# Kernel tuning notes

Hardware: AMD Instinct MI355X
Metric: run time of the kernel (lower is better)

The kernel has to match this reference:

```python
import jax, jax.numpy as jnp
import numpy as np

B, N, D_OBS, D_MSG, H = 4096, 64, 128, 64, 4
HD = D_MSG // H
EPS = 1e-5


def setup_inputs() -> dict:
    key = jax.random.key(0)
    ks = jax.random.split(key, 16)
    def w(k, shape):
        fan_in = shape[0]
        return (jax.random.normal(k, shape, dtype=jnp.float32) / np.sqrt(fan_in)).astype(jnp.float32)
    return {
        'obs_all': jax.random.normal(ks[0], (B, N, D_OBS), dtype=jnp.float32),
        # msg encoder: Linear(obs,128) -> ReLU -> Linear(128,msg)
        'enc_w1': w(ks[1], (D_OBS, 128)), 'enc_b1': jnp.zeros((128,), jnp.float32),
        'enc_w2': w(ks[2], (128, D_MSG)), 'enc_b2': jnp.zeros((D_MSG,), jnp.float32),
        # MultiheadAttention in/out projections (stored as (in, out))
        'in_proj_w': w(ks[3], (D_MSG, 3 * D_MSG)), 'in_proj_b': jnp.zeros((3 * D_MSG,), jnp.float32),
        'out_w': w(ks[4], (D_MSG, D_MSG)), 'out_b': jnp.zeros((D_MSG,), jnp.float32),
        # integrator: Linear(obs+msg,256) -> LayerNorm(256) -> ReLU -> Linear(256,obs)
        'int_w1': w(ks[5], (D_OBS + D_MSG, 256)), 'int_b1': jnp.zeros((256,), jnp.float32),
        'ln_g': jnp.ones((256,), jnp.float32), 'ln_b': jnp.zeros((256,), jnp.float32),
        'int_w2': w(ks[6], (256, D_OBS)), 'int_b2': jnp.zeros((D_OBS,), jnp.float32),
    }


def reference(obs_all, enc_w1, enc_b1, enc_w2, enc_b2,
              in_proj_w, in_proj_b, out_w, out_b,
              int_w1, int_b1, ln_g, ln_b, int_w2, int_b2):
    # --- send: encode observations into messages (B, N, msg_dim) ---
    h = jax.nn.relu(obs_all @ enc_w1 + enc_b1)
    msgs = h @ enc_w2 + enc_b2

    # --- attention aggregation: per-agent query over all messages.
    # The original per-agent loop (query = msgs[:, i:i+1]) is exactly
    # batched self-attention over the agent axis.
    qkv = msgs @ in_proj_w + in_proj_b            # (B, N, 3*msg)
    q, k, v = jnp.split(qkv, 3, axis=-1)
    q = q.reshape(B, N, H, HD)
    k = k.reshape(B, N, H, HD)
    v = v.reshape(B, N, H, HD)
    scale = 1.0 / np.sqrt(HD)
    scores = jnp.einsum('bqhd,bkhd->bhqk', q, k) * scale   # (B, H, N, N)
    attn = jax.nn.softmax(scores, axis=-1)
    ctx = jnp.einsum('bhqk,bkhd->bqhd', attn, v).reshape(B, N, D_MSG)
    agg = ctx @ out_w + out_b                     # (B, N, msg_dim)

    # --- receive: concat obs + aggregated message, MLP with LayerNorm ---
    combined = jnp.concatenate([obs_all, agg], axis=-1)
    z = combined @ int_w1 + int_b1                # (B, N, 256)
    mu = jnp.mean(z, axis=-1, keepdims=True)
    var = jnp.var(z, axis=-1, keepdims=True)
    z = (z - mu) * jax.lax.rsqrt(var + EPS) * ln_g + ln_b
    enriched = jax.nn.relu(z) @ int_w2 + int_b2   # (B, N, obs_dim)
    return enriched, msgs
```

## Files before the change

### kernel.cpp

```cpp
#include <hip/hip_runtime.h>


typedef __attribute__((ext_vector_type(8))) short bf16x8;
typedef __attribute__((ext_vector_type(4))) float f32x4;
typedef __attribute__((ext_vector_type(16))) float f32x16;

#define MFMA16(a, b, c) __builtin_amdgcn_mfma_f32_16x16x32_bf16((a), (b), (c), 0, 0, 0)
#define MFMA32(a, b, c) __builtin_amdgcn_mfma_f32_32x32x16_bf16((a), (b), (c), 0, 0, 0)

__device__ __forceinline__ float b2f(short s) {
    union { unsigned u; float f; } x;
    x.u = ((unsigned)(unsigned short)s) << 16;
    return x.f;
}
__device__ __forceinline__ short f2b(float f) {
    union { float f; unsigned u; } x;
    x.f = f;
    unsigned r = (x.u + 0x7FFFu + ((x.u >> 16) & 1u)) >> 16;
    return (short)r;
}

template<bool F32>
__device__ __forceinline__ float ldS(const void* p, int i) {
    if (F32) return ((const float*)p)[i];
    return b2f(((const short*)p)[i]);
}
template<bool F32>
__device__ __forceinline__ bf16x8 ld8(const void* p, long i) {
    if (F32) {
        const float4* f = (const float4*)((const float*)p + i);
        float4 a = f[0], b = f[1];
        bf16x8 r;
        r[0] = f2b(a.x); r[1] = f2b(a.y); r[2] = f2b(a.z); r[3] = f2b(a.w);
        r[4] = f2b(b.x); r[5] = f2b(b.y); r[6] = f2b(b.z); r[7] = f2b(b.w);
        return r;
    }
    return *(const bf16x8*)((const short*)p + i);
}
template<bool F32>
__device__ __forceinline__ void st(void* p, long i, float v) {
    if (F32) ((float*)p)[i] = v;
    else ((short*)p)[i] = f2b(v);
}

#define P_S   0
#define H_S   0
#define Z_S   0
#define Q2_S  9216
#define AG_S  9216
#define K2_S  13312
#define VT_S  17408
#define LN_S  17408
#define MU_S  18432
#define MS_S  22016
#define SMEM_SHORTS 26624
#define HP 136
#define MP 72
#define ZP 264
#define PP 72
#define VP 72

#define WT1_OFF   0
#define WT2_OFF   16384
#define WTQ_OFF   24576
#define WTO_OFF   36864
#define WTI1_OFF  40960
#define WTI2_OFF  90112

__global__ void detect_dtype(const unsigned short* __restrict__ obs, int* __restrict__ flag) {
    if (blockIdx.x != 0) return;
    int lane = threadIdx.x & 63;
    int cnt = 0;
    for (int i = lane; i < 512; i += 64) {
        unsigned e = (obs[i] >> 7) & 0xFFu;
        cnt += (e == 0u || (e >= 80u && e <= 140u)) ? 1 : 0;
    }
#pragma unroll
    for (int off = 1; off < 64; off <<= 1) cnt += __shfl_xor(cnt, off);
    if (lane == 0) *flag = (cnt >= 480) ? 1 : 0;
}

__global__ void wtrans(const void* __restrict__ w1, const void* __restrict__ w2,
                       const void* __restrict__ wq, const void* __restrict__ wo,
                       const void* __restrict__ wi1, const void* __restrict__ wi2,
                       const int* __restrict__ flag, short* __restrict__ wt) {
    const bool f32 = (*flag == 0);
    int id = blockIdx.x * 256 + threadIdx.x;
    const void* src;
    int K, N, off, loc;
    if (id < 16384)       { src = w1;  K = 128; N = 128; off = WT1_OFF;  loc = id; }
    else if (id < 24576)  { src = w2;  K = 128; N = 64;  off = WT2_OFF;  loc = id - 16384; }
    else if (id < 36864)  { src = wq;  K = 64;  N = 192; off = WTQ_OFF;  loc = id - 24576; }
    else if (id < 40960)  { src = wo;  K = 64;  N = 64;  off = WTO_OFF;  loc = id - 36864; }
    else if (id < 90112)  { src = wi1; K = 192; N = 256; off = WTI1_OFF; loc = id - 40960; }
    else if (id < 122880) { src = wi2; K = 256; N = 128; off = WTI2_OFF; loc = id - 90112; }
    else return;
    int n = loc / K;
    int k = loc - n * K;
    float v = f32 ? ((const float*)src)[k * N + n] : b2f(((const short*)src)[k * N + n]);
    wt[off + loc] = f2b(v);
}

template<bool F32>
__global__ __launch_bounds__(256, 3)
void macs_main(const void* __restrict__ obs,
               const void* __restrict__ eb1, const void* __restrict__ eb2,
               const void* __restrict__ ipb, const void* __restrict__ ob,
               const void* __restrict__ ib1, const void* __restrict__ lg,
               const void* __restrict__ lb,  const void* __restrict__ ib2,
               const int* __restrict__ flag, const short* __restrict__ wt,
               void* __restrict__ out) {
    if (*flag != (F32 ? 0 : 1)) return;
    __shared__ __align__(16) short smem[SMEM_SHORTS];
    const int tid = threadIdx.x;
    const int w = tid >> 6;
    const int lane = tid & 63;
    const int q = lane >> 4;
    const int t = lane & 15;
    const int l31 = lane & 31;
    const int hi = lane >> 5;
    const int b = blockIdx.x;
    const long obase = (long)b * 64 * 128;

    {
        f32x4 acc[4][2] = {};
        const short* wt1 = wt + WT1_OFF;
#pragma unroll
        for (int ks = 0; ks < 4; ++ks) {
            bf16x8 a[4], bb[2];
#pragma unroll
            for (int mt = 0; mt < 4; ++mt)
                a[mt] = ld8<F32>(obs, obase + (mt * 16 + t) * 128 + ks * 32 + q * 8);
#pragma unroll
            for (int tj = 0; tj < 2; ++tj)
                bb[tj] = *(const bf16x8*)(wt1 + (w * 32 + tj * 16 + t) * 128 + ks * 32 + q * 8);
#pragma unroll
            for (int mt = 0; mt < 4; ++mt)
#pragma unroll
                for (int tj = 0; tj < 2; ++tj)
                    acc[mt][tj] = MFMA16(a[mt], bb[tj], acc[mt][tj]);
        }
        short* hs = smem + H_S;
#pragma unroll
        for (int tj = 0; tj < 2; ++tj) {
            int c = w * 32 + tj * 16 + t;
            float bias = ldS<F32>(eb1, c);
#pragma unroll
            for (int mt = 0; mt < 4; ++mt)
#pragma unroll
                for (int i = 0; i < 4; ++i) {
                    int r = mt * 16 + q * 4 + i;
                    hs[r * HP + c] = f2b(fmaxf(acc[mt][tj][i] + bias, 0.f));
                }
        }
    }
    __syncthreads();

    {
        f32x4 acc[4] = {};
        const short* wt2 = wt + WT2_OFF;
        const short* hs = smem + H_S;
#pragma unroll
        for (int ks = 0; ks < 4; ++ks) {
            bf16x8 a[4];
            bf16x8 bb = *(const bf16x8*)(wt2 + (w * 16 + t) * 128 + ks * 32 + q * 8);
#pragma unroll
            for (int mt = 0; mt < 4; ++mt)
                a[mt] = *(const bf16x8*)(hs + (mt * 16 + t) * HP + ks * 32 + q * 8);
#pragma unroll
            for (int mt = 0; mt < 4; ++mt)
                acc[mt] = MFMA16(a[mt], bb, acc[mt]);
        }
        short* ms = smem + MS_S;
        float bias = ldS<F32>(eb2, w * 16 + t);
        const long msgs_base = 33554432L;
#pragma unroll
        for (int mt = 0; mt < 4; ++mt)
#pragma unroll
            for (int i = 0; i < 4; ++i) {
                int r = mt * 16 + q * 4 + i;
                float v = acc[mt][i] + bias;
                ms[r * MP + w * 16 + t] = f2b(v);
                st<F32>(out, msgs_base + ((long)b * 64 + r) * 64 + w * 16 + t, v);
            }
    }
    __syncthreads();

    {
        f32x4 acc[4][3] = {};
        const short* wtq = wt + WTQ_OFF;
        const short* ms = smem + MS_S;
#pragma unroll
        for (int ks = 0; ks < 2; ++ks) {
            bf16x8 a[4], bb[3];
#pragma unroll
            for (int mt = 0; mt < 4; ++mt)
                a[mt] = *(const bf16x8*)(ms + (mt * 16 + t) * MP + ks * 32 + q * 8);
#pragma unroll
            for (int tj = 0; tj < 3; ++tj)
                bb[tj] = *(const bf16x8*)(wtq + (w * 48 + tj * 16 + t) * 64 + ks * 32 + q * 8);
#pragma unroll
            for (int mt = 0; mt < 4; ++mt)
#pragma unroll
                for (int tj = 0; tj < 3; ++tj)
                    acc[mt][tj] = MFMA16(a[mt], bb[tj], acc[mt][tj]);
        }
#pragma unroll
        for (int tj = 0; tj < 3; ++tj) {
            int c = w * 48 + tj * 16 + t;
            float bias = ldS<F32>(ipb, c);
            int sec = c >> 6;
            int head = (c >> 4) & 3;
            float scale = (sec == 0) ? 0.25f : 1.0f;
#pragma unroll
            for (int mt = 0; mt < 4; ++mt)
#pragma unroll
                for (int i = 0; i < 4; ++i) {
                    int r = mt * 16 + q * 4 + i;
                    short bv = f2b((acc[mt][tj][i] + bias) * scale);
                    int idx;
                    if (sec == 0)      idx = Q2_S + head * 1024 + r * 16 + t;
                    else if (sec == 1) idx = K2_S + head * 1024 + r * 16 + t;
                    else               idx = VT_S + head * 1152 + t * VP + r;
                    smem[idx] = bv;
                }
        }
    }
    __syncthreads();

    {
        const int rh = w & 1;
        short* Pq = smem + P_S + w * 2304;
        short* cs = smem + MS_S;
#pragma unroll
        for (int p = 0; p < 2; ++p) {
            const int hd = p * 2 + (w >> 1);
            const short* qh = smem + Q2_S + hd * 1024;
            const short* kh = smem + K2_S + hd * 1024;
            const short* vh = smem + VT_S + hd * 1152;
            f32x16 sc0 = {}, sc1 = {};
            {
                bf16x8 aq  = *(const bf16x8*)(qh + (rh * 32 + l31) * 16 + hi * 8);
                bf16x8 bk0 = *(const bf16x8*)(kh + l31 * 16 + hi * 8);
                bf16x8 bk1 = *(const bf16x8*)(kh + (32 + l31) * 16 + hi * 8);
                sc0 = MFMA32(aq, bk0, sc0);
                sc1 = MFMA32(aq, bk1, sc1);
            }
#pragma unroll
            for (int i = 0; i < 16; ++i) {
                int lr = (i & 3) + 8 * (i >> 2) + 4 * hi;
                float e0 = __expf(sc0[i]);
                float e1 = __expf(sc1[i]);
                float s = e0 + e1;
#pragma unroll
                for (int off = 1; off < 32; off <<= 1) s += __shfl_xor(s, off);
                float inv = 1.f / s;
                Pq[lr * PP + l31]      = f2b(e0 * inv);
                Pq[lr * PP + 32 + l31] = f2b(e1 * inv);
            }
            f32x4 cx[2] = {};
#pragma unroll
            for (int ks = 0; ks < 2; ++ks) {
                bf16x8 bb = *(const bf16x8*)(vh + t * VP + ks * 32 + q * 8);
                bf16x8 a0 = *(const bf16x8*)(Pq + t * PP + ks * 32 + q * 8);
                bf16x8 a1 = *(const bf16x8*)(Pq + (16 + t) * PP + ks * 32 + q * 8);
                cx[0] = MFMA16(a0, bb, cx[0]);
                cx[1] = MFMA16(a1, bb, cx[1]);
            }
#pragma unroll
            for (int mt = 0; mt < 2; ++mt)
#pragma unroll
                for (int i = 0; i < 4; ++i)
                    cs[(rh * 32 + mt * 16 + q * 4 + i) * MP + hd * 16 + t] = f2b(cx[mt][i]);
        }
    }
    __syncthreads();

    {
        f32x4 acc[4] = {};
        const short* wto = wt + WTO_OFF;
        const short* cs = smem + MS_S;
#pragma unroll
        for (int ks = 0; ks < 2; ++ks) {
            bf16x8 a[4];
            bf16x8 bb = *(const bf16x8*)(wto + (w * 16 + t) * 64 + ks * 32 + q * 8);
#pragma unroll
            for (int mt = 0; mt < 4; ++mt)
                a[mt] = *(const bf16x8*)(cs + (mt * 16 + t) * MP + ks * 32 + q * 8);
#pragma unroll
            for (int mt = 0; mt < 4; ++mt)
                acc[mt] = MFMA16(a[mt], bb, acc[mt]);
        }
        short* ag = smem + AG_S;
        float bias = ldS<F32>(ob, w * 16 + t);
#pragma unroll
        for (int mt = 0; mt < 4; ++mt)
#pragma unroll
            for (int i = 0; i < 4; ++i)
                ag[(mt * 16 + q * 4 + i) * MP + w * 16 + t] = f2b(acc[mt][i] + bias);
    }
    __syncthreads();

    {
        f32x4 acc[4][4] = {};
        const short* wti1 = wt + WTI1_OFF;
        const short* ag = smem + AG_S;
#pragma unroll
        for (int ks = 0; ks < 6; ++ks) {
            bf16x8 a[4], bb[4];
            if (ks < 4) {
#pragma unroll
                for (int mt = 0; mt < 4; ++mt)
                    a[mt] = ld8<F32>(obs, obase + (mt * 16 + t) * 128 + ks * 32 + q * 8);
            } else {
#pragma unroll
                for (int mt = 0; mt < 4; ++mt)
                    a[mt] = *(const bf16x8*)(ag + (mt * 16 + t) * MP + (ks - 4) * 32 + q * 8);
            }
#pragma unroll
            for (int tj = 0; tj < 4; ++tj)
                bb[tj] = *(const bf16x8*)(wti1 + (w * 64 + tj * 16 + t) * 192 + ks * 32 + q * 8);
#pragma unroll
            for (int mt = 0; mt < 4; ++mt)
#pragma unroll
                for (int tj = 0; tj < 4; ++tj)
                    acc[mt][tj] = MFMA16(a[mt], bb[tj], acc[mt][tj]);
        }
#pragma unroll
        for (int tj = 0; tj < 4; ++tj) {
            float bias = ldS<F32>(ib1, w * 64 + tj * 16 + t);
#pragma unroll
            for (int mt = 0; mt < 4; ++mt)
#pragma unroll
                for (int i = 0; i < 4; ++i) acc[mt][tj][i] += bias;
        }
        float2* lnred = (float2*)(smem + LN_S);
#pragma unroll
        for (int mt = 0; mt < 4; ++mt)
#pragma unroll
            for (int i = 0; i < 4; ++i) {
                float s = 0.f, s2 = 0.f;
#pragma unroll
                for (int tj = 0; tj < 4; ++tj) {
                    float v = acc[mt][tj][i];
                    s += v;
                    s2 += v * v;
                }
#pragma unroll
                for (int off = 1; off < 16; off <<= 1) {
                    s += __shfl_xor(s, off);
                    s2 += __shfl_xor(s2, off);
                }
                if (t == 0) {
                    float2 p; p.x = s; p.y = s2;
                    lnred[(mt * 16 + q * 4 + i) * 4 + w] = p;
                }
            }
        __syncthreads();
        float2* munr = (float2*)(smem + MU_S);
        if (tid < 64) {
            float S = 0.f, S2 = 0.f;
#pragma unroll
            for (int j = 0; j < 4; ++j) {
                float2 p = lnred[tid * 4 + j];
                S += p.x;
                S2 += p.y;
            }
            float mu = S * (1.f / 256.f);
            float var = S2 * (1.f / 256.f) - mu * mu;
            float2 m; m.x = mu; m.y = rsqrtf(fmaxf(var, 0.f) + 1e-5f);
            munr[tid] = m;
        }
        __syncthreads();
        short* zs = smem + Z_S;
        float gv[4], bv[4];
#pragma unroll
        for (int tj = 0; tj < 4; ++tj) {
            gv[tj] = ldS<F32>(lg, w * 64 + tj * 16 + t);
            bv[tj] = ldS<F32>(lb, w * 64 + tj * 16 + t);
        }
#pragma unroll
        for (int mt = 0; mt < 4; ++mt)
#pragma unroll
            for (int i = 0; i < 4; ++i) {
                int r = mt * 16 + q * 4 + i;
                float2 mr = munr[r];
#pragma unroll
                for (int tj = 0; tj < 4; ++tj) {
                    float v = (acc[mt][tj][i] - mr.x) * mr.y * gv[tj] + bv[tj];
                    zs[r * ZP + w * 64 + tj * 16 + t] = f2b(fmaxf(v, 0.f));
                }
            }
    }
    __syncthreads();

    {
        f32x4 acc[4][2] = {};
        const short* wti2 = wt + WTI2_OFF;
        const short* zs = smem + Z_S;
#pragma unroll
        for (int ks = 0; ks < 8; ++ks) {
            bf16x8 a[4], bb[2];
#pragma unroll
            for (int mt = 0; mt < 4; ++mt)
                a[mt] = *(const bf16x8*)(zs + (mt * 16 + t) * ZP + ks * 32 + q * 8);
#pragma unroll
            for (int tj = 0; tj < 2; ++tj)
                bb[tj] = *(const bf16x8*)(wti2 + (w * 32 + tj * 16 + t) * 256 + ks * 32 + q * 8);
#pragma unroll
            for (int mt = 0; mt < 4; ++mt)
#pragma unroll
                for (int tj = 0; tj < 2; ++tj)
                    acc[mt][tj] = MFMA16(a[mt], bb[tj], acc[mt][tj]);
        }
#pragma unroll
        for (int tj = 0; tj < 2; ++tj) {
            int c = w * 32 + tj * 16 + t;
            float bias = ldS<F32>(ib2, c);
#pragma unroll
            for (int mt = 0; mt < 4; ++mt)
#pragma unroll
                for (int i = 0; i < 4; ++i) {
                    int r = mt * 16 + q * 4 + i;
                    st<F32>(out, ((long)b * 64 + r) * 128 + c, acc[mt][tj][i] + bias);
                }
        }
    }
}

extern "C" void kernel_launch(void* const* d_in, const int* in_sizes, int n_in,
                              void* d_out, int out_size, void* d_ws, size_t ws_size,
                              hipStream_t stream) {
    const void* obs = d_in[0];
    const void* w1  = d_in[1];
    const void* b1  = d_in[2];
    const void* w2  = d_in[3];
    const void* b2  = d_in[4];
    const void* wq  = d_in[5];
    const void* bq  = d_in[6];
    const void* wo  = d_in[7];
    const void* bo  = d_in[8];
    const void* wi1 = d_in[9];
    const void* bi1 = d_in[10];
    const void* lg  = d_in[11];
    const void* lb  = d_in[12];
    const void* wi2 = d_in[13];
    const void* bi2 = d_in[14];
    int* flag = (int*)d_ws;
    short* wt = (short*)d_ws + 128;

    detect_dtype<<<dim3(1), dim3(64), 0, stream>>>((const unsigned short*)obs, flag);
    wtrans<<<dim3(480), dim3(256), 0, stream>>>(w1, w2, wq, wo, wi1, wi2, flag, wt);
    macs_main<false><<<dim3(4096), dim3(256), 0, stream>>>(obs, b1, b2, bq, bo, bi1, lg, lb, bi2, flag, wt, d_out);
    macs_main<true ><<<dim3(4096), dim3(256), 0, stream>>>(obs, b1, b2, bq, bo, bi1, lg, lb, bi2, flag, wt, d_out);
}
```

Measured before the change: 582.5 us.

## Pre-convert fp32 obs to bf16 in workspace, fuse prep kernels, hoist weight loads

Merges dtype detection and weight transposition into one prep kernel, which can also convert the fp32 observation tensor to bf16 in workspace when the workspace is large enough. The main kernel then reads bf16 obs, halving obs traffic on its two reads. It also hoists weight and obs fragment loads ahead of the MFMA loops so more loads are in flight. The trade-off is an extra full pass that reads obs once and writes a bf16 copy, plus higher register pressure under 3-wave occupancy bounds. The conversion path only runs when ws_size is big enough.

```diff
diff --git a/kernel.cpp b/kernel.cpp
--- a/kernel.cpp
+++ b/kernel.cpp
@@ -36,6 +36,11 @@
         return r;
     }
     return *(const bf16x8*)((const short*)p + i);
+}
+template<bool F32, bool OBSBF>
+__device__ __forceinline__ bf16x8 ldobs(const void* obs, const short* obs_bf, long i) {
+    if (OBSBF) return *(const bf16x8*)(obs_bf + i);
+    return ld8<F32>(obs, i);
 }
 template<bool F32>
 __device__ __forceinline__ void st(void* p, long i, float v) {
@@ -66,42 +71,57 @@
 #define WTO_OFF   36864
 #define WTI1_OFF  40960
 #define WTI2_OFF  90112
-
-__global__ void detect_dtype(const unsigned short* __restrict__ obs, int* __restrict__ flag) {
-    if (blockIdx.x != 0) return;
+#define WT_TOTAL  122880
+#define OBS_ELEMS 33554432L
+#define WS_NEEDED (256UL + (unsigned long)WT_TOTAL * 2 + (unsigned long)OBS_ELEMS * 2)
+
+template<bool DO_CONV>
+__global__ void prep(const void* __restrict__ obs,
+                     const void* __restrict__ w1, const void* __restrict__ w2,
+                     const void* __restrict__ wq, const void* __restrict__ wo,
+                     const void* __restrict__ wi1, const void* __restrict__ wi2,
+                     int* __restrict__ flag, short* __restrict__ wt,
+                     short* __restrict__ obs_bf) {
+    const unsigned short* o16 = (const unsigned short*)obs;
     int lane = threadIdx.x & 63;
     int cnt = 0;
     for (int i = lane; i < 512; i += 64) {
-        unsigned e = (obs[i] >> 7) & 0xFFu;
+        unsigned e = (o16[i] >> 7) & 0xFFu;
         cnt += (e == 0u || (e >= 80u && e <= 140u)) ? 1 : 0;
     }
 #pragma unroll
     for (int off = 1; off < 64; off <<= 1) cnt += __shfl_xor(cnt, off);
-    if (lane == 0) *flag = (cnt >= 480) ? 1 : 0;
-}
-
-__global__ void wtrans(const void* __restrict__ w1, const void* __restrict__ w2,
-                       const void* __restrict__ wq, const void* __restrict__ wo,
-                       const void* __restrict__ wi1, const void* __restrict__ wi2,
-                       const int* __restrict__ flag, short* __restrict__ wt) {
-    const bool f32 = (*flag == 0);
-    int id = blockIdx.x * 256 + threadIdx.x;
-    const void* src;
-    int K, N, off, loc;
-    if (id < 16384)       { src = w1;  K = 128; N = 128; off = WT1_OFF;  loc = id; }
-    else if (id < 24576)  { src = w2;  K = 128; N = 64;  off = WT2_OFF;  loc = id - 16384; }
-    else if (id < 36864)  { src = wq;  K = 64;  N = 192; off = WTQ_OFF;  loc = id - 24576; }
-    else if (id < 40960)  { src = wo;  K = 64;  N = 64;  off = WTO_OFF;  loc = id - 36864; }
-    else if (id < 90112)  { src = wi1; K = 192; N = 256; off = WTI1_OFF; loc = id - 40960; }
-    else if (id < 122880) { src = wi2; K = 256; N = 128; off = WTI2_OFF; loc = id - 90112; }
-    else return;
-    int n = loc / K;
-    int k = loc - n * K;
-    float v = f32 ? ((const float*)src)[k * N + n] : b2f(((const short*)src)[k * N + n]);
-    wt[off + loc] = f2b(v);
-}
-
-template<bool F32>
+    const bool isbf16 = (cnt >= 480);
+    if (blockIdx.x == 0 && threadIdx.x == 0) *flag = isbf16 ? 1 : 0;
+
+    long id = (long)blockIdx.x * 256 + threadIdx.x;
+    if (id < WT_TOTAL) {
+        const void* src;
+        int K, N, off, loc = (int)id;
+        if (loc < 16384)      { src = w1;  K = 128; N = 128; off = WT1_OFF; }
+        else if (loc < 24576) { src = w2;  K = 128; N = 64;  off = WT2_OFF;  loc -= 16384; }
+        else if (loc < 36864) { src = wq;  K = 64;  N = 192; off = WTQ_OFF;  loc -= 24576; }
+        else if (loc < 40960) { src = wo;  K = 64;  N = 64;  off = WTO_OFF;  loc -= 36864; }
+        else if (loc < 90112) { src = wi1; K = 192; N = 256; off = WTI1_OFF; loc -= 40960; }
+        else                  { src = wi2; K = 256; N = 128; off = WTI2_OFF; loc -= 90112; }
+        int n = loc / K;
+        int k = loc - n * K;
+        float v = isbf16 ? b2f(((const short*)src)[k * N + n]) : ((const float*)src)[k * N + n];
+        wt[off + loc] = f2b(v);
+    } else if (DO_CONV && !isbf16) {
+        long base = (id - WT_TOTAL) * 8;
+        if (base < OBS_ELEMS) {
+            const float4* f = (const float4*)((const float*)obs + base);
+            float4 a = f[0], b = f[1];
+            bf16x8 r;
+            r[0] = f2b(a.x); r[1] = f2b(a.y); r[2] = f2b(a.z); r[3] = f2b(a.w);
+            r[4] = f2b(b.x); r[5] = f2b(b.y); r[6] = f2b(b.z); r[7] = f2b(b.w);
+            *(bf16x8*)(obs_bf + base) = r;
+        }
+    }
+}
+
+template<bool F32, bool OBSBF>
 __global__ __launch_bounds__(256, 3)
 void macs_main(const void* __restrict__ obs,
                const void* __restrict__ eb1, const void* __restrict__ eb2,
@@ -109,7 +129,7 @@
                const void* __restrict__ ib1, const void* __restrict__ lg,
                const void* __restrict__ lb,  const void* __restrict__ ib2,
                const int* __restrict__ flag, const short* __restrict__ wt,
-               void* __restrict__ out) {
+               const short* __restrict__ obs_bf, void* __restrict__ out) {
     if (*flag != (F32 ? 0 : 1)) return;
     __shared__ __align__(16) short smem[SMEM_SHORTS];
     const int tid = threadIdx.x;
@@ -123,14 +143,17 @@
     const long obase = (long)b * 64 * 128;
 
     {
+        bf16x8 oa[4][4];
+#pragma unroll
+        for (int ks = 0; ks < 4; ++ks)
+#pragma unroll
+            for (int mt = 0; mt < 4; ++mt)
+                oa[ks][mt] = ldobs<F32, OBSBF>(obs, obs_bf, obase + (mt * 16 + t) * 128 + ks * 32 + q * 8);
         f32x4 acc[4][2] = {};
         const short* wt1 = wt + WT1_OFF;
 #pragma unroll
         for (int ks = 0; ks < 4; ++ks) {
-            bf16x8 a[4], bb[2];
-#pragma unroll
-            for (int mt = 0; mt < 4; ++mt)
-                a[mt] = ld8<F32>(obs, obase + (mt * 16 + t) * 128 + ks * 32 + q * 8);
+            bf16x8 bb[2];
 #pragma unroll
             for (int tj = 0; tj < 2; ++tj)
                 bb[tj] = *(const bf16x8*)(wt1 + (w * 32 + tj * 16 + t) * 128 + ks * 32 + q * 8);
@@ -138,7 +161,7 @@
             for (int mt = 0; mt < 4; ++mt)
 #pragma unroll
                 for (int tj = 0; tj < 2; ++tj)
-                    acc[mt][tj] = MFMA16(a[mt], bb[tj], acc[mt][tj]);
+                    acc[mt][tj] = MFMA16(oa[ks][mt], bb[tj], acc[mt][tj]);
         }
         short* hs = smem + H_S;
 #pragma unroll
@@ -157,19 +180,22 @@
     __syncthreads();
 
     {
+        bf16x8 bbv[4];
+        const short* wt2 = wt + WT2_OFF;
+#pragma unroll
+        for (int ks = 0; ks < 4; ++ks)
+            bbv[ks] = *(const bf16x8*)(wt2 + (w * 16 + t) * 128 + ks * 32 + q * 8);
         f32x4 acc[4] = {};
-        const short* wt2 = wt + WT2_OFF;
         const short* hs = smem + H_S;
 #pragma unroll
         for (int ks = 0; ks < 4; ++ks) {
             bf16x8 a[4];
-            bf16x8 bb = *(const bf16x8*)(wt2 + (w * 16 + t) * 128 + ks * 32 + q * 8);
 #pragma unroll
             for (int mt = 0; mt < 4; ++mt)
                 a[mt] = *(const bf16x8*)(hs + (mt * 16 + t) * HP + ks * 32 + q * 8);
 #pragma unroll
             for (int mt = 0; mt < 4; ++mt)
-                acc[mt] = MFMA16(a[mt], bb, acc[mt]);
+                acc[mt] = MFMA16(a[mt], bbv[ks], acc[mt]);
         }
         short* ms = smem + MS_S;
         float bias = ldS<F32>(eb2, w * 16 + t);
@@ -187,23 +213,26 @@
     __syncthreads();
 
     {
+        bf16x8 bbv[6];
+        const short* wtq = wt + WTQ_OFF;
+#pragma unroll
+        for (int ks = 0; ks < 2; ++ks)
+#pragma unroll
+            for (int tj = 0; tj < 3; ++tj)
+                bbv[ks * 3 + tj] = *(const bf16x8*)(wtq + (w * 48 + tj * 16 + t) * 64 + ks * 32 + q * 8);
         f32x4 acc[4][3] = {};
-        const short* wtq = wt + WTQ_OFF;
         const short* ms = smem + MS_S;
 #pragma unroll
         for (int ks = 0; ks < 2; ++ks) {
-            bf16x8 a[4], bb[3];
+            bf16x8 a[4];
 #pragma unroll
             for (int mt = 0; mt < 4; ++mt)
                 a[mt] = *(const bf16x8*)(ms + (mt * 16 + t) * MP + ks * 32 + q * 8);
 #pragma unroll
-            for (int tj = 0; tj < 3; ++tj)
-                bb[tj] = *(const bf16x8*)(wtq + (w * 48 + tj * 16 + t) * 64 + ks * 32 + q * 8);
-#pragma unroll
             for (int mt = 0; mt < 4; ++mt)
 #pragma unroll
                 for (int tj = 0; tj < 3; ++tj)
-                    acc[mt][tj] = MFMA16(a[mt], bb[tj], acc[mt][tj]);
+                    acc[mt][tj] = MFMA16(a[mt], bbv[ks * 3 + tj], acc[mt][tj]);
         }
 #pragma unroll
         for (int tj = 0; tj < 3; ++tj) {
@@ -276,20 +305,29 @@
     }
     __syncthreads();
 
-    {
+    bf16x8 oa6[4][4];
+    {
+#pragma unroll
+        for (int ks = 0; ks < 4; ++ks)
+#pragma unroll
+            for (int mt = 0; mt < 4; ++mt)
+                oa6[ks][mt] = ldobs<F32, OBSBF>(obs, obs_bf, obase + (mt * 16 + t) * 128 + ks * 32 + q * 8);
+        bf16x8 bbv[2];
+        const short* wto = wt + WTO_OFF;
+#pragma unroll
+        for (int ks = 0; ks < 2; ++ks)
+            bbv[ks] = *(const bf16x8*)(wto + (w * 16 + t) * 64 + ks * 32 + q * 8);
         f32x4 acc[4] = {};
-        const short* wto = wt + WTO_OFF;
         const short* cs = smem + MS_S;
 #pragma unroll
         for (int ks = 0; ks < 2; ++ks) {
             bf16x8 a[4];
-            bf16x8 bb = *(const bf16x8*)(wto + (w * 16 + t) * 64 + ks * 32 + q * 8);
 #pragma unroll
             for (int mt = 0; mt < 4; ++mt)
                 a[mt] = *(const bf16x8*)(cs + (mt * 16 + t) * MP + ks * 32 + q * 8);
 #pragma unroll
             for (int mt = 0; mt < 4; ++mt)
-                acc[mt] = MFMA16(a[mt], bb, acc[mt]);
+                acc[mt] = MFMA16(a[mt], bbv[ks], acc[mt]);
         }
         short* ag = smem + AG_S;
         float bias = ldS<F32>(ob, w * 16 + t);
@@ -311,7 +349,7 @@
             if (ks < 4) {
 #pragma unroll
                 for (int mt = 0; mt < 4; ++mt)
-                    a[mt] = ld8<F32>(obs, obase + (mt * 16 + t) * 128 + ks * 32 + q * 8);
+                    a[mt] = oa6[ks][mt];
             } else {
 #pragma unroll
                 for (int mt = 0; mt < 4; ++mt)
@@ -395,23 +433,26 @@
     __syncthreads();
 
     {
+        bf16x8 bbv[8][2];
+        const short* wti2 = wt + WTI2_OFF;
+#pragma unroll
+        for (int ks = 0; ks < 8; ++ks)
+#pragma unroll
+            for (int tj = 0; tj < 2; ++tj)
+                bbv[ks][tj] = *(const bf16x8*)(wti2 + (w * 32 + tj * 16 + t) * 256 + ks * 32 + q * 8);
         f32x4 acc[4][2] = {};
-        const short* wti2 = wt + WTI2_OFF;
         const short* zs = smem + Z_S;
 #pragma unroll
         for (int ks = 0; ks < 8; ++ks) {
-            bf16x8 a[4], bb[2];
+            bf16x8 a[4];
 #pragma unroll
             for (int mt = 0; mt < 4; ++mt)
                 a[mt] = *(const bf16x8*)(zs + (mt * 16 + t) * ZP + ks * 32 + q * 8);
 #pragma unroll
-            for (int tj = 0; tj < 2; ++tj)
-                bb[tj] = *(const bf16x8*)(wti2 + (w * 32 + tj * 16 + t) * 256 + ks * 32 + q * 8);
-#pragma unroll
             for (int mt = 0; mt < 4; ++mt)
 #pragma unroll
                 for (int tj = 0; tj < 2; ++tj)
-                    acc[mt][tj] = MFMA16(a[mt], bb[tj], acc[mt][tj]);
+                    acc[mt][tj] = MFMA16(a[mt], bbv[ks][tj], acc[mt][tj]);
         }
 #pragma unroll
         for (int tj = 0; tj < 2; ++tj) {
@@ -448,9 +489,16 @@
     const void* bi2 = d_in[14];
     int* flag = (int*)d_ws;
     short* wt = (short*)d_ws + 128;
-
-    detect_dtype<<<dim3(1), dim3(64), 0, stream>>>((const unsigned short*)obs, flag);
-    wtrans<<<dim3(480), dim3(256), 0, stream>>>(w1, w2, wq, wo, wi1, wi2, flag, wt);
-    macs_main<false><<<dim3(4096), dim3(256), 0, stream>>>(obs, b1, b2, bq, bo, bi1, lg, lb, bi2, flag, wt, d_out);
-    macs_main<true ><<<dim3(4096), dim3(256), 0, stream>>>(obs, b1, b2, bq, bo, bi1, lg, lb, bi2, flag, wt, d_out);
-}
+    short* obs_bf = (short*)d_ws + 128 + WT_TOTAL;
+    const bool big_ws = (ws_size >= WS_NEEDED);
+
+    if (big_ws) {
+        prep<true><<<dim3(16864), dim3(256), 0, stream>>>(obs, w1, w2, wq, wo, wi1, wi2, flag, wt, obs_bf);
+        macs_main<false, false><<<dim3(4096), dim3(256), 0, stream>>>(obs, b1, b2, bq, bo, bi1, lg, lb, bi2, flag, wt, obs_bf, d_out);
+        macs_main<true,  true ><<<dim3(4096), dim3(256), 0, stream>>>(obs, b1, b2, bq, bo, bi1, lg, lb, bi2, flag, wt, obs_bf, d_out);
+    } else {
+        prep<false><<<dim3(480), dim3(256), 0, stream>>>(obs, w1, w2, wq, wo, wi1, wi2, flag, wt, obs_bf);
+        macs_main<false, false><<<dim3(4096), dim3(256), 0, stream>>>(obs, b1, b2, bq, bo, bi1, lg, lb, bi2, flag, wt, obs_bf, d_out);
+        macs_main<true,  false><<<dim3(4096), dim3(256), 0, stream>>>(obs, b1, b2, bq, bo, bi1, lg, lb, bi2, flag, wt, obs_bf, d_out);
+    }
+}
```

After: 586.7 us. Within noise of the previous version (+0.7%).
